# Kernel optimization log

Measured on AMD Instinct MI355X. Metric: run time of the kernel, lower is better.

Reference implementation:

```python
import jax, jax.numpy as jnp
import numpy as np

# ---- static config (matches init_kwargs) ----
D_MODEL = 2048
D_STATE = 64
D_CONV = 4
EXPAND = 2
HEADDIM = 64
NGROUPS = 1
CHUNK = 256
D_INNER = EXPAND * D_MODEL            # 4096
NHEADS = D_INNER // HEADDIM           # 64
CONV_DIM = D_INNER + 2 * NGROUPS * D_STATE   # 4224
D_IN_PROJ = 2 * D_INNER + 2 * NGROUPS * D_STATE + NHEADS  # 8384
EPS = 1e-5


def setup_inputs() -> dict:
    key = jax.random.key(0)
    ks = jax.random.split(key, 7)
    B, L = 2, 2048
    u = jax.random.normal(ks[0], (B, L, D_MODEL), jnp.float32)
    W_in = jax.random.normal(ks[1], (D_IN_PROJ, D_MODEL), jnp.float32) * (D_MODEL ** -0.5)
    conv_w = jax.random.normal(ks[2], (CONV_DIM, D_CONV), jnp.float32) * (D_CONV ** -0.5)
    conv_b = jnp.zeros((CONV_DIM,), jnp.float32)
    # dt_bias = softplus^{-1}(dt) with dt ~ LogUniform(1e-3, 1e-1), as in the torch init
    dt = jnp.exp(jax.random.uniform(ks[3], (NHEADS,), jnp.float32)
                 * (np.log(0.1) - np.log(0.001)) + np.log(0.001))
    dt_bias = dt + jnp.log(-jnp.expm1(-dt))
    A_log = jnp.log(jax.random.uniform(ks[4], (NHEADS,), jnp.float32, minval=1.0, maxval=16.0))
    D = jnp.ones((NHEADS,), jnp.float32)
    norm_w = jnp.ones((D_INNER,), jnp.float32)
    W_out = jax.random.normal(ks[5], (D_MODEL, D_INNER), jnp.float32) * (D_INNER ** -0.5)
    return dict(u=u, W_in=W_in, conv_w=conv_w, conv_b=conv_b, dt_bias=dt_bias,
                A_log=A_log, D=D, norm_w=norm_w, W_out=W_out)


def _chunked_ssd(x, dt, A, Bm, Cm):
    """Mamba2 chunked selective scan (ssd, discrete form).
    x:[b,l,h,p] dt:[b,l,h] A:[h] Bm,Cm:[b,l,n] (ngroups=1, broadcast over heads).
    Returns y:[b,l,h,p]."""
    b, l, h, p = x.shape
    c = l // CHUNK
    xc = x.reshape(b, c, CHUNK, h, p)
    dtc = dt.reshape(b, c, CHUNK, h)
    Bc = Bm.reshape(b, c, CHUNK, D_STATE)
    Cc = Cm.reshape(b, c, CHUNK, D_STATE)

    Abar = (dtc * A).transpose(0, 3, 1, 2)          # [b,h,c,s]
    Acum = jnp.cumsum(Abar, axis=-1)                # [b,h,c,s]

    # intra-chunk decay matrix L[i,j] = exp(sum_{k=j+1..i} Abar_k), lower-tri
    seg = Acum[..., :, None] - Acum[..., None, :]   # [b,h,c,s,s]
    tri = jnp.tril(jnp.ones((CHUNK, CHUNK), bool))
    Lmat = jnp.where(tri, jnp.exp(seg), 0.0)

    xdt = xc * dtc[..., None]                       # [b,c,s,h,p] (dt*B*x discretization)
    Y_diag = jnp.einsum('bcln,bcsn,bhcls,bcshp->bclhp', Cc, Bc, Lmat, xdt)

    # per-chunk final states
    decay_states = jnp.exp(Acum[..., -1:] - Acum)   # [b,h,c,s]
    states = jnp.einsum('bcsn,bhcs,bcshp->bchpn', Bc, decay_states, xdt)

    # inter-chunk recurrence (associative scan across chunk summaries)
    Achunk = Acum[..., -1]                          # [b,h,c]
    Acs = jnp.cumsum(jnp.pad(Achunk, ((0, 0), (0, 0), (1, 0))), axis=-1)  # [b,h,c+1]
    segc = Acs[..., :, None] - Acs[..., None, :]
    tric = jnp.tril(jnp.ones((c + 1, c + 1), bool))
    decay_chunk = jnp.where(tric, jnp.exp(segc), 0.0)          # [b,h,c+1,c+1]
    states0 = jnp.pad(states, ((0, 0), (1, 0), (0, 0), (0, 0), (0, 0)))  # zero init state
    new_states = jnp.einsum('bhzc,bchpn->bzhpn', decay_chunk, states0)
    prev_states = new_states[:, :-1]                # state entering each chunk [b,c,h,p,n]

    state_decay = jnp.exp(Acum)                     # [b,h,c,s]
    Y_off = jnp.einsum('bcln,bchpn,bhcl->bclhp', Cc, prev_states, state_decay)
    return (Y_diag + Y_off).reshape(b, l, h, p)


def reference(u, W_in, conv_w, conv_b, dt_bias, A_log, D, norm_w, W_out):
    b, l, _ = u.shape
    zxbcdt = u @ W_in.T                                        # [b,l,8384]
    z = zxbcdt[..., :D_INNER]
    xBC = zxbcdt[..., D_INNER:D_INNER + CONV_DIM]
    dt = jax.nn.softplus(zxbcdt[..., D_INNER + CONV_DIM:] + dt_bias)  # [b,l,h]

    # causal depthwise conv1d + SiLU
    xp = jnp.pad(xBC, ((0, 0), (D_CONV - 1, 0), (0, 0)))
    xBC = conv_b + sum(xp[:, w:w + l, :] * conv_w[:, w] for w in range(D_CONV))
    xBC = jax.nn.silu(xBC)

    x = xBC[..., :D_INNER].reshape(b, l, NHEADS, HEADDIM)
    Bm = xBC[..., D_INNER:D_INNER + D_STATE]
    Cm = xBC[..., D_INNER + D_STATE:]

    A = -jnp.exp(A_log)                                        # [h]
    y = _chunked_ssd(x, dt, A, Bm, Cm)                         # [b,l,h,p]
    y = y + x * D[None, None, :, None]                         # D skip on raw x
    y = y.reshape(b, l, D_INNER)

    # gated RMSNorm (norm_before_gate=False): gate first, then normalize
    y = y * jax.nn.silu(z)
    y = y * jax.lax.rsqrt(jnp.mean(y * y, axis=-1, keepdims=True) + EPS) * norm_w
    return y @ W_out.T
```

## Files before the change

### kernel.cpp

```cpp
#include <hip/hip_runtime.h>
#include <hip/hip_bf16.h>
#include <cstdint>

#define DPROJ  8384

typedef __attribute__((ext_vector_type(8))) short short8;
typedef __attribute__((ext_vector_type(4))) short sh4;
typedef __attribute__((ext_vector_type(4))) float f32x4;

#define ZX_OFF     0ul
#define DTB_OFF    34340864ul
#define ACU_OFF    34603008ul
#define CBT_OFF    34865152ul
#define ST_OFF     36175872ul
#define YB_OFF     40370176ul
#define HALO_OFF   57147392ul
#define U16_OFF    40370176ul
#define WIN16_OFF  48758784ul
#define WOUT16_OFF 34340864ul

__device__ __forceinline__ short f2bf(float x) {
  union { float f; uint32_t u; } v{x};
  uint32_t r = (v.u + 0x7fff + ((v.u >> 16) & 1)) >> 16;
  return (short)r;
}
__device__ __forceinline__ float bf2f(short s) {
  union { uint32_t u; float f; } v;
  v.u = ((uint32_t)(uint16_t)s) << 16;
  return v.f;
}

__global__ __launch_bounds__(256) void cast_bf16_kernel(
    const float* __restrict__ in, short* __restrict__ out, int n8) {
  int i = blockIdx.x * 256 + threadIdx.x;
  if (i >= n8) return;
  const float4* p = (const float4*)(in + (size_t)i * 8);
  float4 a = p[0], b = p[1];
  short8 o;
  o[0] = f2bf(a.x); o[1] = f2bf(a.y); o[2] = f2bf(a.z); o[3] = f2bf(a.w);
  o[4] = f2bf(b.x); o[5] = f2bf(b.y); o[6] = f2bf(b.z); o[7] = f2bf(b.w);
  *(short8*)(out + (size_t)i * 8) = o;
}

__device__ __forceinline__ void gload16(const void* g, const void* l) {
  __builtin_amdgcn_global_load_lds(
      (const __attribute__((address_space(1))) void*)g,
      (__attribute__((address_space(3))) void*)l, 16, 0, 0);
}

__global__ __launch_bounds__(256) void gemm_bf16(
    const short* __restrict__ A, int lda, const short* __restrict__ B, int ldb,
    float* __restrict__ C, int ldc, int K, int Nvalid) {
  const int orig = blockIdx.x + gridDim.x * blockIdx.y;
  const int xcd = orig & 7;
  const int cid = orig >> 3;
  const int rpx = gridDim.y >> 3;
  const int tn = cid / rpx;
  const int tm = xcd * rpx + (cid % rpx);
  __shared__ __align__(16) short As[128 * 32];
  __shared__ __align__(16) short Bs[128 * 32];
  const int t = threadIdx.x;
  const int w = t >> 6, lane = t & 63;
  const int m0 = tm * 128, n0 = tn * 128;
  const int wr = (w >> 1) * 64, wc = (w & 1) * 64;
  const int arow = t >> 2, kk = (t & 3) * 8;
  const int fr = lane & 15, fk = (lane >> 4) * 8;
  int br0 = n0 + arow;       if (br0 > Nvalid - 1) br0 = Nvalid - 1;
  int br1 = n0 + 64 + arow;  if (br1 > Nvalid - 1) br1 = Nvalid - 1;
  const short* pa0 = A + (size_t)(m0 + arow) * lda + kk;
  const short* pa1 = A + (size_t)(m0 + 64 + arow) * lda + kk;
  const short* pb0 = B + (size_t)br0 * ldb + kk;
  const short* pb1 = B + (size_t)br1 * ldb + kk;
  short* la = As + w * 512;
  short* lb = Bs + w * 512;
  f32x4 acc[4][4];
#pragma unroll
  for (int i = 0; i < 4; ++i)
#pragma unroll
    for (int j = 0; j < 4; ++j) acc[i][j] = (f32x4){0.f, 0.f, 0.f, 0.f};

  for (int k0 = 0; k0 < K; k0 += 32) {
    gload16(pa0 + k0, la);
    gload16(pa1 + k0, la + 2048);
    gload16(pb0 + k0, lb);
    gload16(pb1 + k0, lb + 2048);
    __syncthreads();
    short8 af[4], bg[4];
#pragma unroll
    for (int i = 0; i < 4; ++i) {
      af[i] = *(const short8*)&As[(wr + i * 16 + fr) * 32 + fk];
      bg[i] = *(const short8*)&Bs[(wc + i * 16 + fr) * 32 + fk];
    }
#pragma unroll
    for (int i = 0; i < 4; ++i)
#pragma unroll
      for (int j = 0; j < 4; ++j)
        acc[i][j] = __builtin_amdgcn_mfma_f32_16x16x32_bf16(af[i], bg[j],
                                                            acc[i][j], 0, 0, 0);
    __syncthreads();
  }
#pragma unroll
  for (int i = 0; i < 4; ++i) {
    const int row = m0 + wr + i * 16 + (lane >> 4) * 4;
#pragma unroll
    for (int j = 0; j < 4; ++j) {
      const int col = n0 + wc + j * 16 + fr;
      if (col < Nvalid) {
#pragma unroll
        for (int r = 0; r < 4; ++r)
          C[(size_t)(row + r) * ldc + col] = acc[i][j][r];
      }
    }
  }
}

__global__ __launch_bounds__(256) void halo_kernel(const float* __restrict__ zx,
                                                   float* __restrict__ halo) {
  int idx = blockIdx.x * 256 + threadIdx.x;
  int ch = idx % 4224;
  int r = idx / 4224;
  int j = r % 3;
  int r2 = r / 3;
  int lc = r2 & 15, b = r2 >> 4;
  int l = lc * 128 - 3 + j;
  halo[idx] = (l < 0) ? 0.f : zx[(size_t)(b * 2048 + l) * DPROJ + 4096 + ch];
}

__global__ __launch_bounds__(256) void conv_kernel(float* __restrict__ zx,
                                                   const float* __restrict__ halo,
                                                   const float* __restrict__ cw,
                                                   const float* __restrict__ cb) {
  int idx = blockIdx.x * 256 + threadIdx.x;
  int ch = idx % 4224;
  int r = idx / 4224;
  int lc = r & 15, b = r >> 4;
  float w0 = cw[ch * 4 + 0], w1 = cw[ch * 4 + 1], w2 = cw[ch * 4 + 2],
        w3 = cw[ch * 4 + 3];
  float bias = cb[ch];
  const float* hp = halo + (size_t)r * 3 * 4224 + ch;
  float x3 = hp[0], x2 = hp[4224], x1 = hp[2 * 4224];
  size_t base = (size_t)(b * 2048 + lc * 128) * DPROJ + 4096 + ch;
  for (int i = 0; i < 128; ++i) {
    float x0 = zx[base];
    float v = bias + w0 * x3 + w1 * x2 + w2 * x1 + w3 * x0;
    v = v / (1.f + __expf(-v));
    zx[base] = v;
    x3 = x2; x2 = x1; x1 = x0;
    base += DPROJ;
  }
}

__global__ __launch_bounds__(256) void dtacum_kernel(
    const float* __restrict__ zx, const float* __restrict__ dt_bias,
    const float* __restrict__ A_log, float* __restrict__ dtb,
    float* __restrict__ acu) {
  int bid = blockIdx.x;
  int c = bid & 7, h = (bid >> 3) & 63, b = bid >> 9;
  int s = threadIdx.x;
  int tok = b * 2048 + c * 256 + s;
  float raw = zx[(size_t)tok * DPROJ + 8320 + h] + dt_bias[h];
  float dtv = (raw > 20.f) ? raw : log1pf(expf(raw));
  float A = -expf(A_log[h]);
  __shared__ float sc[256];
  sc[s] = dtv * A;
  __syncthreads();
  for (int off = 1; off < 256; off <<= 1) {
    float v = (s >= off) ? sc[s - off] : 0.f;
    __syncthreads();
    sc[s] += v;
    __syncthreads();
  }
  int o = (b * 64 + h) * 2048 + c * 256 + s;
  dtb[o] = dtv;
  acu[o] = sc[s];
}

__global__ __launch_bounds__(256) void cbt_kernel(const float* __restrict__ zx,
                                                  short* __restrict__ cbtT) {
  __shared__ float cl[256][33];
  __shared__ float blds[16][32];
  int bid = blockIdx.x;
  int sb = bid & 15, c = (bid >> 4) & 7, b = bid >> 7;
  int t = threadIdx.x;
  int tok0 = b * 2048 + c * 256;
  float acc[16];
#pragma unroll
  for (int i = 0; i < 16; ++i) acc[i] = 0.f;
  for (int nh = 0; nh < 2; ++nh) {
    __syncthreads();
    for (int it = 0; it < 32; ++it) {
      int e = it * 256 + t;
      int row = e >> 5, n = e & 31;
      cl[row][n] = zx[(size_t)(tok0 + row) * DPROJ + 8256 + nh * 32 + n];
    }
    for (int it = 0; it < 2; ++it) {
      int e = it * 256 + t;
      int row = e >> 5, n = e & 31;
      blds[row][n] =
          zx[(size_t)(tok0 + sb * 16 + row) * DPROJ + 8192 + nh * 32 + n];
    }
    __syncthreads();
    for (int n = 0; n < 32; ++n) {
      float cv = cl[t][n];
#pragma unroll
      for (int s2 = 0; s2 < 16; ++s2) acc[s2] += cv * blds[s2][n];
    }
  }
  short* outp = cbtT + ((size_t)(b * 8 + c) * 256 + t) * 256 + sb * 16;
#pragma unroll
  for (int s2 = 0; s2 < 16; ++s2) outp[s2] = f2bf(acc[s2]);
}

__global__ __launch_bounds__(256) void states_mfma(
    const float* __restrict__ zx, const float* __restrict__ dtb,
    const float* __restrict__ acu, float* __restrict__ st) {
  __shared__ __align__(16) short As2[64][136];
  __shared__ __align__(16) short Bs2[64][136];
  __shared__ float wl[256];
  int bid = blockIdx.x;
  int h = bid & 63, c = (bid >> 6) & 7, b = bid >> 9;
  int t = threadIdx.x;
  int w = t >> 6, lane = t & 63;
  int tok0 = b * 2048 + c * 256;
  int bh = (b * 64 + h) * 2048 + c * 256;
  {
    float aend = acu[bh + 255];
    wl[t] = __expf(aend - acu[bh + t]) * dtb[bh + t];
  }
  __syncthreads();
  const float* xbase = zx + (size_t)tok0 * DPROJ + 4096 + h * 64;
  const float* bbase = zx + (size_t)tok0 * DPROJ + 8192;
  const int fr = lane & 15, fko = (lane >> 4) * 8;
  const int wi = (w >> 1) * 32, wj = (w & 1) * 32;
  f32x4 acc[2][2];
#pragma unroll
  for (int i = 0; i < 2; ++i)
#pragma unroll
    for (int j = 0; j < 2; ++j) acc[i][j] = (f32x4){0.f, 0.f, 0.f, 0.f};

  for (int ph = 0; ph < 2; ++ph) {
    const int kb = ph * 128;
    if (ph) __syncthreads();
    for (int it = 0; it < 8; ++it) {
      int idx = it * 256 + t;
      int p = idx & 63, kg = idx >> 6;
      int k = kb + kg * 4;
      const float* xp = xbase + (size_t)k * DPROJ + p;
      const float* bp = bbase + (size_t)k * DPROJ + p;
      sh4 oa, ob;
#pragma unroll
      for (int r = 0; r < 4; ++r) {
        oa[r] = f2bf(xp[(size_t)r * DPROJ]);
        ob[r] = f2bf(bp[(size_t)r * DPROJ] * wl[k + r]);
      }
      *(sh4*)&As2[p][kg * 4] = oa;
      *(sh4*)&Bs2[p][kg * 4] = ob;
    }
    __syncthreads();
#pragma unroll
    for (int kk0 = 0; kk0 < 128; kk0 += 32) {
      short8 af[2], bg[2];
#pragma unroll
      for (int i = 0; i < 2; ++i) {
        af[i] = *(const short8*)&As2[wi + i * 16 + fr][kk0 + fko];
        bg[i] = *(const short8*)&Bs2[wj + i * 16 + fr][kk0 + fko];
      }
#pragma unroll
      for (int i = 0; i < 2; ++i)
#pragma unroll
        for (int j = 0; j < 2; ++j)
          acc[i][j] = __builtin_amdgcn_mfma_f32_16x16x32_bf16(af[i], bg[j],
                                                              acc[i][j], 0, 0, 0);
    }
  }
  float* out = st + ((size_t)(b * 8 + c) * 64 + h) * 4096;
  const int rq = (lane >> 4) * 4;
#pragma unroll
  for (int i = 0; i < 2; ++i) {
    int p0 = wi + i * 16 + rq;
#pragma unroll
    for (int j = 0; j < 2; ++j) {
      int n = wj + j * 16 + fr;
#pragma unroll
      for (int r = 0; r < 4; ++r)
        out[(size_t)(p0 + r) * 64 + n] = acc[i][j][r];
    }
  }
}

__global__ __launch_bounds__(256) void chunkscan_kernel(
    const float* __restrict__ acu, float* __restrict__ st) {
  int bid = blockIdx.x;
  int pc = bid & 15, h = (bid >> 4) & 63, b = bid >> 10;
  int pn = pc * 256 + threadIdx.x;
  int abase = (b * 64 + h) * 2048;
  float run = 0.f;
  for (int c = 0; c < 8; ++c) {
    size_t idx = ((size_t)(b * 8 + c) * 64 + h) * 4096 + pn;
    float s = st[idx];
    st[idx] = run;
    float ach = acu[abase + c * 256 + 255];
    run = run * __expf(ach) + s;
  }
}

__global__ __launch_bounds__(256) void ydiag_mfma(
    const float* __restrict__ zx, const float* __restrict__ dtb,
    const float* __restrict__ acu, const short* __restrict__ cbtT,
    const float* __restrict__ st, const float* __restrict__ Dp,
    float* __restrict__ yb) {
  __shared__ __align__(16) short Xs[64][328];
  __shared__ float acs[256];
  __shared__ float dts[256];
  int bid = blockIdx.x;
  int h = bid & 63, c = (bid >> 6) & 7, b = bid >> 9;
  int t = threadIdx.x;
  int w = t >> 6, lane = t & 63;
  int tok0 = b * 2048 + c * 256;
  int bh = (b * 64 + h) * 2048 + c * 256;
  acs[t] = acu[bh + t];
  dts[t] = dtb[bh + t];
  const float* xbase = zx + (size_t)tok0 * DPROJ + 4096 + h * 64;
  const float* st_b = st + ((size_t)(b * 8 + c) * 64 + h) * 4096;
  for (int it = 0; it < 16; ++it) {
    int idx = it * 256 + t;
    int p = idx & 63, kg = idx >> 6;
    const float* xp = xbase + (size_t)(kg * 4) * DPROJ + p;
    sh4 o;
    o[0] = f2bf(xp[0]);
    o[1] = f2bf(xp[DPROJ]);
    o[2] = f2bf(xp[2 * DPROJ]);
    o[3] = f2bf(xp[3 * DPROJ]);
    *(sh4*)&Xs[p][kg * 4] = o;
  }
  for (int it = 0; it < 4; ++it) {
    int idx = it * 256 + t;
    int ng = idx & 15, p = idx >> 4;
    float4 v = *(const float4*)&st_b[p * 64 + ng * 4];
    sh4 o;
    o[0] = f2bf(v.x); o[1] = f2bf(v.y); o[2] = f2bf(v.z); o[3] = f2bf(v.w);
    *(sh4*)&Xs[p][256 + ng * 4] = o;
  }
  __syncthreads();

  const int fr = lane & 15, fko = (lane >> 4) * 8;
  const int wr = w * 64;
  float Al[4], eAl[4];
#pragma unroll
  for (int i = 0; i < 4; ++i) {
    Al[i] = acs[wr + i * 16 + fr];
    eAl[i] = __expf(Al[i]);
  }
  f32x4 acc[4][4];
#pragma unroll
  for (int i = 0; i < 4; ++i)
#pragma unroll
    for (int j = 0; j < 4; ++j) acc[i][j] = (f32x4){0.f, 0.f, 0.f, 0.f};

  const short* cbt_b = cbtT + (size_t)(b * 8 + c) * 65536;

  for (int k0 = 0; k0 < wr + 64; k0 += 32) {
    short8 bg[4];
#pragma unroll
    for (int j = 0; j < 4; ++j)
      bg[j] = *(const short8*)&Xs[j * 16 + fr][k0 + fko];
    const int bi = (k0 + 32 < 256) ? (k0 + 32) : 255;
    const float base = acs[bi];
    float vd[8];
#pragma unroll
    for (int jj = 0; jj < 8; ++jj) {
      int s = k0 + fko + jj;
      vd[jj] = __expf(base - acs[s]) * dts[s];
    }
#pragma unroll
    for (int i = 0; i < 4; ++i) {
      const int li0 = wr + i * 16;
      if (k0 > li0 + 15) continue;
      const int l = li0 + fr;
      const short8 cb = *(const short8*)&cbt_b[(size_t)l * 256 + k0 + fko];
      short8 af;
      if (k0 + 32 <= li0) {
        const float u = __expf(Al[i] - base);
#pragma unroll
        for (int jj = 0; jj < 8; ++jj)
          af[jj] = f2bf(bf2f(cb[jj]) * (vd[jj] * u));
      } else {
#pragma unroll
        for (int jj = 0; jj < 8; ++jj) {
          int s = k0 + fko + jj;
          float wv = 0.f;
          if (s <= l) wv = bf2f(cb[jj]) * __expf(Al[i] - acs[s]) * dts[s];
          af[jj] = f2bf(wv);
        }
      }
#pragma unroll
      for (int j = 0; j < 4; ++j)
        acc[i][j] = __builtin_amdgcn_mfma_f32_16x16x32_bf16(af, bg[j],
                                                            acc[i][j], 0, 0, 0);
    }
  }
#pragma unroll
  for (int k0 = 256; k0 < 320; k0 += 32) {
    short8 bg[4];
#pragma unroll
    for (int j = 0; j < 4; ++j)
      bg[j] = *(const short8*)&Xs[j * 16 + fr][k0 + fko];
#pragma unroll
    for (int i = 0; i < 4; ++i) {
      const int l = wr + i * 16 + fr;
      const float* cr =
          zx + (size_t)(tok0 + l) * DPROJ + 8256 + (k0 - 256) + fko;
      float4 c0 = *(const float4*)cr;
      float4 c1 = *(const float4*)(cr + 4);
      short8 af;
      af[0] = f2bf(c0.x * eAl[i]); af[1] = f2bf(c0.y * eAl[i]);
      af[2] = f2bf(c0.z * eAl[i]); af[3] = f2bf(c0.w * eAl[i]);
      af[4] = f2bf(c1.x * eAl[i]); af[5] = f2bf(c1.y * eAl[i]);
      af[6] = f2bf(c1.z * eAl[i]); af[7] = f2bf(c1.w * eAl[i]);
#pragma unroll
      for (int j = 0; j < 4; ++j)
        acc[i][j] = __builtin_amdgcn_mfma_f32_16x16x32_bf16(af, bg[j],
                                                            acc[i][j], 0, 0, 0);
    }
  }
  float Dh = Dp[h];
  const int rq = (lane >> 4) * 4;
#pragma unroll
  for (int i = 0; i < 4; ++i) {
    int l0 = wr + i * 16 + rq;
#pragma unroll
    for (int j = 0; j < 4; ++j) {
      int p = j * 16 + fr;
      sh4 x4 = *(const sh4*)&Xs[p][l0];
      f32x4 a = acc[i][j];
#pragma unroll
      for (int r = 0; r < 4; ++r)
        yb[(size_t)(bh + l0 + r) * 64 + p] = a[r] + Dh * bf2f(x4[r]);
    }
  }
}

__global__ __launch_bounds__(256) void gatenorm_kernel(
    const float* zx, const float* __restrict__ nw,
    const float* __restrict__ yb, short* ybh) {
  int tok = blockIdx.x;
  int b = tok >> 11, l = tok & 2047;
  int t = threadIdx.x;
  float g[16];
  float ss = 0.f;
#pragma unroll
  for (int i = 0; i < 16; ++i) {
    int d = i * 256 + t;
    int h = d >> 6, p = d & 63;
    float yv = yb[((size_t)(b * 64 + h) * 2048 + l) * 64 + p];
    float zv = zx[(size_t)tok * DPROJ + d];
    float gv = yv * (zv / (1.f + __expf(-zv)));
    g[i] = gv;
    ss += gv * gv;
  }
  for (int off = 32; off > 0; off >>= 1) ss += __shfl_down(ss, off);
  __shared__ float red[4];
  int wid = t >> 6, lane = t & 63;
  if (lane == 0) red[wid] = ss;
  __syncthreads();
  float tot = red[0] + red[1] + red[2] + red[3];
  float scale = rsqrtf(tot * (1.f / 4096.f) + 1e-5f);
#pragma unroll
  for (int i = 0; i < 16; ++i) {
    int d = i * 256 + t;
    ybh[(size_t)tok * 16768 + d] = f2bf(g[i] * scale * nw[d]);
  }
}

extern "C" void kernel_launch(void* const* d_in, const int* in_sizes, int n_in,
                              void* d_out, int out_size, void* d_ws,
                              size_t ws_size, hipStream_t stream) {
  const float* u = (const float*)d_in[0];
  const float* W_in = (const float*)d_in[1];
  const float* conv_w = (const float*)d_in[2];
  const float* conv_b = (const float*)d_in[3];
  const float* dt_bias = (const float*)d_in[4];
  const float* A_log = (const float*)d_in[5];
  const float* Dp = (const float*)d_in[6];
  const float* norm_w = (const float*)d_in[7];
  const float* W_out = (const float*)d_in[8];
  float* out = (float*)d_out;
  float* ws = (float*)d_ws;

  float* zx = ws + ZX_OFF;
  float* dtb = ws + DTB_OFF;
  float* acu = ws + ACU_OFF;
  short* cbtT = (short*)(ws + CBT_OFF);
  float* st = ws + ST_OFF;
  float* yb = ws + YB_OFF;
  float* halo = ws + HALO_OFF;
  short* u16 = (short*)(ws + U16_OFF);
  short* win16 = (short*)(ws + WIN16_OFF);
  short* wout16 = (short*)(ws + WOUT16_OFF);
  short* ybh = (short*)zx;

  cast_bf16_kernel<<<4096, 256, 0, stream>>>(u, u16, 1048576);
  cast_bf16_kernel<<<8384, 256, 0, stream>>>(W_in, win16, 2146304);
  gemm_bf16<<<dim3(66, 32), 256, 0, stream>>>(u16, 2048, win16, 2048, zx, DPROJ,
                                              2048, DPROJ);
  halo_kernel<<<1584, 256, 0, stream>>>(zx, halo);
  conv_kernel<<<528, 256, 0, stream>>>(zx, halo, conv_w, conv_b);
  dtacum_kernel<<<1024, 256, 0, stream>>>(zx, dt_bias, A_log, dtb, acu);
  cbt_kernel<<<256, 256, 0, stream>>>(zx, cbtT);
  states_mfma<<<1024, 256, 0, stream>>>(zx, dtb, acu, st);
  chunkscan_kernel<<<2048, 256, 0, stream>>>(acu, st);
  ydiag_mfma<<<1024, 256, 0, stream>>>(zx, dtb, acu, cbtT, st, Dp, yb);
  cast_bf16_kernel<<<4096, 256, 0, stream>>>(W_out, wout16, 1048576);
  gatenorm_kernel<<<4096, 256, 0, stream>>>(zx, norm_w, yb, ybh);
  gemm_bf16<<<dim3(16, 32), 256, 0, stream>>>(ybh, 16768, wout16, 4096, out,
                                              2048, 4096, 2048);
}
```

Measured before the change: 514.5 us.

## Replace input-projection GEMM with 256x256-tile, 8-wave double-buffered pipelined kernel

Adds a new bf16 MFMA GEMM for the input projection that uses 256x256 output tiles, 512 threads (8 waves), a K-step of 64 split into two halves, and double-buffered LDS fed by direct global-to-LDS loads. Loads for the next K tile are interleaved with MFMA work, with setprio raised around the MFMA bursts and an XOR swizzle applied to the LDS layout. The larger tile is meant to raise arithmetic intensity and hide load latency. In exchange it uses 128KB of LDS per block and more registers, and launches only 528 blocks, which may leave the wave tail unbalanced.

```diff
diff --git a/kernel.cpp b/kernel.cpp
--- a/kernel.cpp
+++ b/kernel.cpp
@@ -46,6 +46,121 @@
   __builtin_amdgcn_global_load_lds(
       (const __attribute__((address_space(1))) void*)g,
       (__attribute__((address_space(3))) void*)l, 16, 0, 0);
+}
+
+__global__ __launch_bounds__(512, 2) void gemm_8ph(
+    const short* __restrict__ A, int lda, const short* __restrict__ B, int ldb,
+    float* __restrict__ C, int ldc, int K, int Nvalid) {
+  __shared__ __align__(16) short Al[2][2][8192];
+  __shared__ __align__(16) short Bl[2][2][8192];
+  const int t = threadIdx.x;
+  const int w = t >> 6, lane = t & 63;
+  const int wm = w >> 2, wn = w & 3;
+  const int fr = lane & 15, fko = (lane >> 4) * 8;
+  const int orig = blockIdx.x + gridDim.x * blockIdx.y;
+  const int xcd = orig & 7, cid = orig >> 3, rpx = gridDim.y >> 3;
+  const int tn = cid / rpx, tm = xcd * rpx + cid % rpx;
+  const int m0 = tm * 256, n0 = tn * 256;
+  const int sr = lane >> 2;
+  const int sck = (lane & 3) * 8;
+
+  f32x4 acc[8][4];
+#pragma unroll
+  for (int i = 0; i < 8; ++i)
+#pragma unroll
+    for (int j = 0; j < 4; ++j) acc[i][j] = (f32x4){0.f, 0.f, 0.f, 0.f};
+
+  const int nt = K >> 6;
+
+#define STAGE_A(kt, hh, dd)                                                    \
+  {                                                                            \
+    _Pragma("unroll") for (int c = 0; c < 2; ++c) {                            \
+      int r_ = c * 128 + w * 16 + sr;                                          \
+      int ks_ = (kt)*64 + (hh)*32 + (sck ^ ((r_ & 3) << 3));                   \
+      gload16(A + (size_t)(m0 + r_) * lda + ks_,                               \
+              &Al[dd][hh][c * 4096 + w * 512 + lane * 8]);                     \
+    }                                                                          \
+  }
+#define STAGE_B(kt, hh, dd)                                                    \
+  {                                                                            \
+    _Pragma("unroll") for (int c = 0; c < 2; ++c) {                            \
+      int r_ = c * 128 + w * 16 + sr;                                          \
+      int br_ = n0 + r_;                                                       \
+      if (br_ > Nvalid - 1) br_ = Nvalid - 1;                                  \
+      int ks_ = (kt)*64 + (hh)*32 + (sck ^ ((r_ & 3) << 3));                   \
+      gload16(B + (size_t)br_ * ldb + ks_,                                     \
+              &Bl[dd][hh][c * 4096 + w * 512 + lane * 8]);                     \
+    }                                                                          \
+  }
+#define LOAD_BG(dd, hh, BG)                                                    \
+  _Pragma("unroll") for (int j = 0; j < 4; ++j) {                              \
+    int r_ = wn * 64 + j * 16 + fr;                                            \
+    BG[j] = *(const short8*)&Bl[dd][hh][r_ * 32 + (fko ^ ((r_ & 3) << 3))];    \
+  }
+#define COMPUTE4(dd, hh, I0, BG)                                               \
+  {                                                                            \
+    short8 af_[4];                                                             \
+    _Pragma("unroll") for (int ii = 0; ii < 4; ++ii) {                         \
+      int r_ = wm * 128 + ((I0) + ii) * 16 + fr;                               \
+      af_[ii] = *(const short8*)&Al[dd][hh][r_ * 32 + (fko ^ ((r_ & 3) << 3))];\
+    }                                                                          \
+    __builtin_amdgcn_s_setprio(1);                                             \
+    _Pragma("unroll") for (int ii = 0; ii < 4; ++ii)                           \
+        _Pragma("unroll") for (int j = 0; j < 4; ++j)                          \
+            acc[(I0) + ii][j] = __builtin_amdgcn_mfma_f32_16x16x32_bf16(       \
+                af_[ii], BG[j], acc[(I0) + ii][j], 0, 0, 0);                   \
+    __builtin_amdgcn_s_setprio(0);                                             \
+  }
+
+  STAGE_A(0, 0, 0);
+  STAGE_B(0, 0, 0);
+  STAGE_A(0, 1, 0);
+  STAGE_B(0, 1, 0);
+  asm volatile("s_waitcnt vmcnt(4)" ::: "memory");
+  __builtin_amdgcn_s_barrier();
+
+  int d = 0;
+  for (int kt = 0; kt < nt; ++kt, d ^= 1) {
+    const int nk = (kt + 1 < nt) ? kt + 1 : 0;
+    STAGE_A(nk, 0, d ^ 1);
+    {
+      short8 bg[4];
+      LOAD_BG(d, 0, bg);
+      COMPUTE4(d, 0, 0, bg);
+      STAGE_B(nk, 0, d ^ 1);
+      COMPUTE4(d, 0, 4, bg);
+    }
+    asm volatile("s_waitcnt vmcnt(4)" ::: "memory");
+    __builtin_amdgcn_s_barrier();
+    STAGE_A(nk, 1, d ^ 1);
+    {
+      short8 bg[4];
+      LOAD_BG(d, 1, bg);
+      COMPUTE4(d, 1, 0, bg);
+      STAGE_B(nk, 1, d ^ 1);
+      COMPUTE4(d, 1, 4, bg);
+    }
+    asm volatile("s_waitcnt vmcnt(4)" ::: "memory");
+    __builtin_amdgcn_s_barrier();
+  }
+#undef STAGE_A
+#undef STAGE_B
+#undef LOAD_BG
+#undef COMPUTE4
+
+#pragma unroll
+  for (int i = 0; i < 8; ++i) {
+    const int row = m0 + wm * 128 + i * 16 + (lane >> 4) * 4;
+#pragma unroll
+    for (int j = 0; j < 4; ++j) {
+      const int col = n0 + wn * 64 + j * 16 + fr;
+      if (col < Nvalid) {
+#pragma unroll
+        for (int r = 0; r < 4; ++r)
+          C[(size_t)(row + r) * ldc + col] = acc[i][j][r];
+      }
+    }
+  }
 }
 
 __global__ __launch_bounds__(256) void gemm_bf16(
@@ -501,8 +616,8 @@
 
   cast_bf16_kernel<<<4096, 256, 0, stream>>>(u, u16, 1048576);
   cast_bf16_kernel<<<8384, 256, 0, stream>>>(W_in, win16, 2146304);
-  gemm_bf16<<<dim3(66, 32), 256, 0, stream>>>(u16, 2048, win16, 2048, zx, DPROJ,
-                                              2048, DPROJ);
+  gemm_8ph<<<dim3(33, 16), 512, 0, stream>>>(u16, 2048, win16, 2048, zx, DPROJ,
+                                             2048, DPROJ);
   halo_kernel<<<1584, 256, 0, stream>>>(zx, halo);
   conv_kernel<<<528, 256, 0, stream>>>(zx, halo, conv_w, conv_b);
   dtacum_kernel<<<1024, 256, 0, stream>>>(zx, dt_bias, A_log, dtb, acu);
```

Measured after the change: 530.5 us. +3.1%, slower.

## Replace input-projection GEMM with 256x256 tile, 8-wave double-buffered bf16 kernel

Applied to the files above, without the earlier changes.

Adds a new GEMM kernel with 256x256 output tiles, 512 threads (8 waves), K-step 64, double-buffered LDS filled via global_load_lds with an XOR swizzle, and s_setprio around the MFMA bursts. It is used for the large input projection GEMM instead of the 128x128 kernel. The intent is more operand reuse per LDS load and overlap of global loads with MFMA compute. In exchange it uses 128KB of LDS per block and many accumulator registers, which limits occupancy. The grid also becomes coarse (528 blocks), which may leave CUs poorly balanced.

```diff
diff --git a/kernel.cpp b/kernel.cpp
--- a/kernel.cpp
+++ b/kernel.cpp
@@ -46,6 +46,97 @@
   __builtin_amdgcn_global_load_lds(
       (const __attribute__((address_space(1))) void*)g,
       (__attribute__((address_space(3))) void*)l, 16, 0, 0);
+}
+
+__global__ __launch_bounds__(512, 2) void gemm_8ph(
+    const short* __restrict__ A, int lda, const short* __restrict__ B, int ldb,
+    float* __restrict__ C, int ldc, int K, int Nvalid) {
+  __shared__ __align__(16) short Al[2][16384];
+  __shared__ __align__(16) short Bl[2][16384];
+  const int t = threadIdx.x;
+  const int w = t >> 6, lane = t & 63;
+  const int wm = w >> 2, wn = w & 3;
+  const int fr = lane & 15, fko = (lane >> 4) * 8;
+  const int orig = blockIdx.x + gridDim.x * blockIdx.y;
+  const int xcd = orig & 7, cid = orig >> 3, rpx = gridDim.y >> 3;
+  const int tn = cid / rpx, tm = xcd * rpx + cid % rpx;
+  const int m0 = tm * 256, n0 = tn * 256;
+  const int sr = lane >> 2;
+  const int sck = (lane & 3) * 8;
+
+  f32x4 acc[8][4];
+#pragma unroll
+  for (int i = 0; i < 8; ++i)
+#pragma unroll
+    for (int j = 0; j < 4; ++j) acc[i][j] = (f32x4){0.f, 0.f, 0.f, 0.f};
+
+  const int nt = K >> 6;
+
+#define SWZ(r_) ((((r_) >> 1) & 3) << 3)
+#define STAGE_TILE(kt, dd)                                                     \
+  {                                                                            \
+    _Pragma("unroll") for (int hh = 0; hh < 2; ++hh)                           \
+        _Pragma("unroll") for (int c = 0; c < 2; ++c) {                        \
+      int r_ = c * 128 + w * 16 + sr;                                          \
+      int ks_ = (kt)*64 + hh * 32 + (sck ^ SWZ(r_));                           \
+      int br_ = n0 + r_;                                                       \
+      if (br_ > Nvalid - 1) br_ = Nvalid - 1;                                  \
+      int dst_ = hh * 8192 + c * 4096 + w * 512 + lane * 8;                    \
+      gload16(A + (size_t)(m0 + r_) * lda + ks_, &Al[dd][dst_]);               \
+      gload16(B + (size_t)br_ * ldb + ks_, &Bl[dd][dst_]);                     \
+    }                                                                          \
+  }
+#define COMPUTE_HALF(dd, hh)                                                   \
+  {                                                                            \
+    short8 bg_[4];                                                             \
+    _Pragma("unroll") for (int j = 0; j < 4; ++j) {                            \
+      int r_ = wn * 64 + j * 16 + fr;                                          \
+      bg_[j] = *(const short8*)&Bl[dd][hh * 8192 + r_ * 32 + (fko ^ SWZ(r_))]; \
+    }                                                                          \
+    _Pragma("unroll") for (int io = 0; io < 2; ++io) {                         \
+      short8 af_[4];                                                           \
+      _Pragma("unroll") for (int ii = 0; ii < 4; ++ii) {                       \
+        int r_ = wm * 128 + (io * 4 + ii) * 16 + fr;                           \
+        af_[ii] =                                                              \
+            *(const short8*)&Al[dd][hh * 8192 + r_ * 32 + (fko ^ SWZ(r_))];    \
+      }                                                                        \
+      __builtin_amdgcn_s_setprio(1);                                           \
+      _Pragma("unroll") for (int ii = 0; ii < 4; ++ii)                         \
+          _Pragma("unroll") for (int j = 0; j < 4; ++j)                        \
+              acc[io * 4 + ii][j] = __builtin_amdgcn_mfma_f32_16x16x32_bf16(   \
+                  af_[ii], bg_[j], acc[io * 4 + ii][j], 0, 0, 0);              \
+      __builtin_amdgcn_s_setprio(0);                                           \
+    }                                                                          \
+  }
+
+  STAGE_TILE(0, 0);
+  int d = 0;
+  for (int kt = 0; kt < nt; ++kt, d ^= 1) {
+    const int nk = (kt + 1 < nt) ? kt + 1 : 0;
+    STAGE_TILE(nk, d ^ 1);
+    asm volatile("s_waitcnt vmcnt(8)" ::: "memory");
+    __builtin_amdgcn_s_barrier();
+    COMPUTE_HALF(d, 0);
+    COMPUTE_HALF(d, 1);
+    __builtin_amdgcn_s_barrier();
+  }
+#undef SWZ
+#undef STAGE_TILE
+#undef COMPUTE_HALF
+
+#pragma unroll
+  for (int i = 0; i < 8; ++i) {
+    const int row = m0 + wm * 128 + i * 16 + (lane >> 4) * 4;
+#pragma unroll
+    for (int j = 0; j < 4; ++j) {
+      const int col = n0 + wn * 64 + j * 16 + fr;
+      if (col < Nvalid) {
+#pragma unroll
+        for (int r = 0; r < 4; ++r)
+          C[(size_t)(row + r) * ldc + col] = acc[i][j][r];
+      }
+    }
+  }
 }
 
 __global__ __launch_bounds__(256) void gemm_bf16(
@@ -501,8 +592,8 @@
 
   cast_bf16_kernel<<<4096, 256, 0, stream>>>(u, u16, 1048576);
   cast_bf16_kernel<<<8384, 256, 0, stream>>>(W_in, win16, 2146304);
-  gemm_bf16<<<dim3(66, 32), 256, 0, stream>>>(u16, 2048, win16, 2048, zx, DPROJ,
-                                              2048, DPROJ);
+  gemm_8ph<<<dim3(33, 16), 512, 0, stream>>>(u16, 2048, win16, 2048, zx, DPROJ,
+                                             2048, DPROJ);
   halo_kernel<<<1584, 256, 0, stream>>>(zx, halo);
   conv_kernel<<<528, 256, 0, stream>>>(zx, halo, conv_w, conv_b);
   dtacum_kernel<<<1024, 256, 0, stream>>>(zx, dt_bias, A_log, dtb, acu);
```

Result: no change. 514.3 us (-0.0%).

## Triple-buffer LDS in bf16 GEMM with async prefetch and XOR swizzle

Applied to the files above, without the earlier changes.

The GEMM main loop now keeps three LDS stages and issues global-to-LDS loads two k-tiles ahead. It waits on vmcnt instead of running a full syncthreads before each compute step, so memory latency overlaps the MFMA work. It also XOR-swizzles the k offset per row pair, on both the global source address and the LDS read, to cut LDS bank conflicts. This triples LDS use per block, which may lower occupancy. The loop also issues dummy loads of tile 0 near the end.

```diff
diff --git a/kernel.cpp b/kernel.cpp
--- a/kernel.cpp
+++ b/kernel.cpp
@@ -57,39 +57,55 @@
   const int rpx = gridDim.y >> 3;
   const int tn = cid / rpx;
   const int tm = xcd * rpx + (cid % rpx);
-  __shared__ __align__(16) short As[128 * 32];
-  __shared__ __align__(16) short Bs[128 * 32];
+  __shared__ __align__(16) short As[3][4096];
+  __shared__ __align__(16) short Bs[3][4096];
   const int t = threadIdx.x;
   const int w = t >> 6, lane = t & 63;
   const int m0 = tm * 128, n0 = tn * 128;
   const int wr = (w >> 1) * 64, wc = (w & 1) * 64;
   const int arow = t >> 2, kk = (t & 3) * 8;
   const int fr = lane & 15, fk = (lane >> 4) * 8;
+  const int swz = ((arow >> 1) & 3) << 3;
   int br0 = n0 + arow;       if (br0 > Nvalid - 1) br0 = Nvalid - 1;
   int br1 = n0 + 64 + arow;  if (br1 > Nvalid - 1) br1 = Nvalid - 1;
-  const short* pa0 = A + (size_t)(m0 + arow) * lda + kk;
-  const short* pa1 = A + (size_t)(m0 + 64 + arow) * lda + kk;
-  const short* pb0 = B + (size_t)br0 * ldb + kk;
-  const short* pb1 = B + (size_t)br1 * ldb + kk;
-  short* la = As + w * 512;
-  short* lb = Bs + w * 512;
+  const short* pa0 = A + (size_t)(m0 + arow) * lda + (kk ^ swz);
+  const short* pa1 = A + (size_t)(m0 + 64 + arow) * lda + (kk ^ swz);
+  const short* pb0 = B + (size_t)br0 * ldb + (kk ^ swz);
+  const short* pb1 = B + (size_t)br1 * ldb + (kk ^ swz);
   f32x4 acc[4][4];
 #pragma unroll
   for (int i = 0; i < 4; ++i)
 #pragma unroll
     for (int j = 0; j < 4; ++j) acc[i][j] = (f32x4){0.f, 0.f, 0.f, 0.f};
 
-  for (int k0 = 0; k0 < K; k0 += 32) {
-    gload16(pa0 + k0, la);
-    gload16(pa1 + k0, la + 2048);
-    gload16(pb0 + k0, lb);
-    gload16(pb1 + k0, lb + 2048);
-    __syncthreads();
+  const int nt = K >> 5;
+
+#define STAGE(kt, bb)                                                          \
+  {                                                                            \
+    const int ko_ = (kt) << 5;                                                 \
+    gload16(pa0 + ko_, &As[bb][w * 512]);                                      \
+    gload16(pa1 + ko_, &As[bb][2048 + w * 512]);                               \
+    gload16(pb0 + ko_, &Bs[bb][w * 512]);                                      \
+    gload16(pb1 + ko_, &Bs[bb][2048 + w * 512]);                               \
+  }
+
+  STAGE(0, 0);
+  STAGE(1, 1);
+  asm volatile("s_waitcnt vmcnt(4)" ::: "memory");
+  __builtin_amdgcn_s_barrier();
+  __builtin_amdgcn_sched_barrier(0);
+
+  int cb = 0, sb = 2;
+  for (int kt = 0; kt < nt; ++kt) {
+    const int nk = (kt + 2 < nt) ? kt + 2 : 0;
+    STAGE(nk, sb);
     short8 af[4], bg[4];
 #pragma unroll
     for (int i = 0; i < 4; ++i) {
-      af[i] = *(const short8*)&As[(wr + i * 16 + fr) * 32 + fk];
-      bg[i] = *(const short8*)&Bs[(wc + i * 16 + fr) * 32 + fk];
+      const int ra = wr + i * 16 + fr;
+      const int rb = wc + i * 16 + fr;
+      af[i] = *(const short8*)&As[cb][ra * 32 + (fk ^ (((ra >> 1) & 3) << 3))];
+      bg[i] = *(const short8*)&Bs[cb][rb * 32 + (fk ^ (((rb >> 1) & 3) << 3))];
     }
 #pragma unroll
     for (int i = 0; i < 4; ++i)
@@ -97,8 +113,16 @@
       for (int j = 0; j < 4; ++j)
         acc[i][j] = __builtin_amdgcn_mfma_f32_16x16x32_bf16(af[i], bg[j],
                                                             acc[i][j], 0, 0, 0);
-    __syncthreads();
-  }
+    asm volatile("s_waitcnt lgkmcnt(0)" ::: "memory");
+    __builtin_amdgcn_sched_barrier(0);
+    asm volatile("s_waitcnt vmcnt(4)" ::: "memory");
+    __builtin_amdgcn_s_barrier();
+    __builtin_amdgcn_sched_barrier(0);
+    cb = (cb == 2) ? 0 : cb + 1;
+    sb = (sb == 2) ? 0 : sb + 1;
+  }
+#undef STAGE
+
 #pragma unroll
   for (int i = 0; i < 4; ++i) {
     const int row = m0 + wr + i * 16 + (lane >> 4) * 4;
```

Result: slower. 534.4 us (+3.9%).
